# Optimization experiments

Measured on AMD Instinct MI355X. Metric: run time of the kernel, lower is better.

## Reference

```python
import jax, jax.numpy as jnp
import numpy as np

DEPTH, E, F, H, U, I, B = 12, 256, 128, 8, 1000, 1000, 64
HD = E // H  # head dim = 32
N = 2 * F + 1  # seq len = 257


def _ln(x, g, b, eps=1e-5):
    m = jnp.mean(x, axis=-1, keepdims=True)
    v = jnp.var(x, axis=-1, keepdims=True)
    return (x - m) / jnp.sqrt(v + eps) * g + b


def setup_inputs() -> dict:
    key = jax.random.key(0)
    ks = jax.random.split(key, 16)
    s = 0.02  # weight scale for numeric sanity
    inp = {
        "user": jax.random.randint(ks[0], (B, 1), 0, U, dtype=jnp.int64) if jax.config.jax_enable_x64 else jax.random.randint(ks[0], (B, 1), 0, U).astype(jnp.int32),
        "item": jax.random.randint(ks[1], (B, 1), 0, I).astype(jnp.int32),
        "user_table": jax.random.normal(ks[2], (E, U, F), jnp.float32) * s,
        "item_table": jax.random.normal(ks[3], (E, I, F), jnp.float32) * s,
        "cls_token": jax.random.normal(ks[4], (1, 1, E), jnp.float32),
        "positions": jax.random.normal(ks[5], (N, E), jnp.float32) * s,
        "ln1_g": jnp.ones((DEPTH, E), jnp.float32),
        "ln1_b": jnp.zeros((DEPTH, E), jnp.float32),
        "Wq": jax.random.normal(ks[6], (DEPTH, E, E), jnp.float32) * s,
        "bq": jnp.zeros((DEPTH, E), jnp.float32),
        "Wk": jax.random.normal(ks[7], (DEPTH, E, E), jnp.float32) * s,
        "bk": jnp.zeros((DEPTH, E), jnp.float32),
        "Wv": jax.random.normal(ks[8], (DEPTH, E, E), jnp.float32) * s,
        "bv": jnp.zeros((DEPTH, E), jnp.float32),
        "Wo": jax.random.normal(ks[9], (DEPTH, E, E), jnp.float32) * s,
        "bo": jnp.zeros((DEPTH, E), jnp.float32),
        "ln2_g": jnp.ones((DEPTH, E), jnp.float32),
        "ln2_b": jnp.zeros((DEPTH, E), jnp.float32),
        "W1": jax.random.normal(ks[10], (DEPTH, E, 4 * E), jnp.float32) * s,
        "b1": jnp.zeros((DEPTH, 4 * E), jnp.float32),
        "W2": jax.random.normal(ks[11], (DEPTH, 4 * E, E), jnp.float32) * s,
        "b2": jnp.zeros((DEPTH, E), jnp.float32),
        "head_g": jnp.ones((E,), jnp.float32),
        "head_b": jnp.zeros((E,), jnp.float32),
        "head_W": jax.random.normal(ks[12], (E, 1), jnp.float32) * s,
        "head_bias": jnp.zeros((1,), jnp.float32),
    }
    return inp


def _forward(user, item, user_table, item_table, cls_token, positions,
             ln1_g, ln1_b, Wq, bq, Wk, bk, Wv, bv, Wo, bo,
             ln2_g, ln2_b, W1, b1, W2, b2, head_g, head_b, head_W, head_bias):
    uid = user[:, 0]
    iid = item[:, 0]
    b = uid.shape[0]
    # emb_size parallel embedding lookups, cat over table axis, then transpose:
    # x_user[b, f, e] = user_table[e, uid[b], f]  -> (b, F, E)
    xu = jnp.transpose(user_table[:, uid, :], (1, 2, 0))
    xi = jnp.transpose(item_table[:, iid, :], (1, 2, 0))
    cls = jnp.broadcast_to(cls_token, (b, 1, E))
    x = jnp.concatenate([cls, xu, xi], axis=1) + positions  # (b, N, E)

    def block(x, p):
        g1, be1, wq, bq_, wk, bk_, wv, bv_, wo, bo_, g2, be2, w1, bb1, w2, bb2 = p
        h = _ln(x, g1, be1)

        def heads(w, bias):
            y = h @ w + bias  # (b, N, E)
            return y.reshape(b, N, H, HD).transpose(0, 2, 1, 3)  # (b, H, N, HD)

        q, k, v = heads(wq, bq_), heads(wk, bk_), heads(wv, bv_)
        energy = jnp.einsum('bhqd,bhkd->bhqk', q, k)  # NOTE: unscaled pre-softmax
        att = jax.nn.softmax(energy, axis=-1) / jnp.sqrt(jnp.float32(E))  # post-softmax scaling quirk
        o = jnp.einsum('bhqk,bhkd->bhqd', att, v)
        o = o.transpose(0, 2, 1, 3).reshape(b, N, E)
        x = x + (o @ wo + bo_)
        h2 = _ln(x, g2, be2)
        ff = jax.nn.gelu(h2 @ w1 + bb1, approximate=False) @ w2 + bb2
        return x + ff, None

    x, _ = jax.lax.scan(block, x, (ln1_g, ln1_b, Wq, bq, Wk, bk, Wv, bv, Wo, bo,
                                   ln2_g, ln2_b, W1, b1, W2, b2))
    pooled = jnp.mean(x, axis=1)  # (b, E)
    return _ln(pooled, head_g, head_b) @ head_W + head_bias  # (b, 1)


def reference(user, item, user_table, item_table, cls_token, positions,
              ln1_g, ln1_b, Wq, bq, Wk, bk, Wv, bv, Wo, bo,
              ln2_g, ln2_b, W1, b1, W2, b2, head_g, head_b, head_W, head_bias):
    return _forward(user, item, user_table, item_table, cls_token, positions,
                    ln1_g, ln1_b, Wq, bq, Wk, bk, Wv, bv, Wo, bo,
                    ln2_g, ln2_b, W1, b1, W2, b2, head_g, head_b, head_W, head_bias)
```

## Files before the change

### kernel.cpp

```cpp
#include <hip/hip_runtime.h>
#include <hip/hip_fp16.h>
#include <math.h>

constexpr int DEPTH = 12;
constexpr int E     = 256;
constexpr int H     = 8;
constexpr int HD    = 32;
constexpr int N     = 257;
constexpr int B     = 64;
constexpr int BN    = B * N;
constexpr int FFD   = 1024;
constexpr int UCNT  = 1000;
constexpr int Fdim  = 128;

enum { EPI_RESID = 1, EPI_GELU = 2, EPI_QKV = 3 };

typedef _Float16 f16x8 __attribute__((ext_vector_type(8)));
typedef _Float16 f16x4 __attribute__((ext_vector_type(4)));
typedef float    f32x4 __attribute__((ext_vector_type(4)));

__device__ __forceinline__ float gelu_exact(float z) {
  return 0.5f * z * (1.0f + erff(z * 0.70710678118654752440f));
}

__global__ __launch_bounds__(128) void embed_kernel(
    const int* __restrict__ user, const int* __restrict__ item,
    const float* __restrict__ utab, const float* __restrict__ itab,
    const float* __restrict__ cls, const float* __restrict__ pos,
    float* __restrict__ x)
{
  const int e = blockIdx.x;
  const int b = blockIdx.y;
  const int f = threadIdx.x;
  const int uid = user[b];
  const int iid = item[b];
  const float uu = utab[((size_t)e * UCNT + uid) * Fdim + f];
  const float ii = itab[((size_t)e * UCNT + iid) * Fdim + f];
  x[((size_t)b * N + 1 + f) * E + e]        = uu + pos[(1 + f) * E + e];
  x[((size_t)b * N + 1 + Fdim + f) * E + e] = ii + pos[(1 + Fdim + f) * E + e];
  if (f == 0) x[((size_t)b * N) * E + e] = cls[e] + pos[e];
}

__global__ __launch_bounds__(256) void convT_kernel(
    const float* __restrict__ in, __half* __restrict__ out,
    int K, int NC, int NCtot, int ncoff)
{
  __shared__ float tile[32][33];
  const int tx = threadIdx.x, ty = threadIdx.y;
  const int n0 = blockIdx.x * 32, k0 = blockIdx.y * 32;
  const float* ip = in + (size_t)blockIdx.z * K * NC;
  __half* op = out + (size_t)blockIdx.z * NCtot * K;
#pragma unroll
  for (int r = 0; r < 4; ++r) {
    const int kk = ty + r * 8;
    tile[kk][tx] = ip[(size_t)(k0 + kk) * NC + n0 + tx];
  }
  __syncthreads();
#pragma unroll
  for (int r = 0; r < 4; ++r) {
    const int nn = ty + r * 8;
    op[(size_t)(ncoff + n0 + nn) * K + k0 + tx] = __float2half(tile[tx][nn]);
  }
}

__global__ __launch_bounds__(256) void ln_kernel(
    const float* __restrict__ x, __half* __restrict__ y,
    const float* __restrict__ g, const float* __restrict__ b)
{
  const int wave = threadIdx.x >> 6, lane = threadIdx.x & 63;
  const int row  = blockIdx.x * 4 + wave;
  const float4 v = *(const float4*)(x + (size_t)row * E + lane * 4);
  float s = v.x + v.y + v.z + v.w;
  float q = v.x * v.x + v.y * v.y + v.z * v.z + v.w * v.w;
#pragma unroll
  for (int o = 32; o > 0; o >>= 1) { s += __shfl_xor(s, o); q += __shfl_xor(q, o); }
  const float mean = s * (1.0f / 256.0f);
  const float var  = q * (1.0f / 256.0f) - mean * mean;
  const float rstd = rsqrtf(var + 1e-5f);
  const float4 gg = *(const float4*)(g + lane * 4);
  const float4 bb = *(const float4*)(b + lane * 4);
  __half2 h0 = __floats2half2_rn((v.x - mean) * rstd * gg.x + bb.x,
                                 (v.y - mean) * rstd * gg.y + bb.y);
  __half2 h1 = __floats2half2_rn((v.z - mean) * rstd * gg.z + bb.z,
                                 (v.w - mean) * rstd * gg.w + bb.w);
  __half2* yp = (__half2*)(y + (size_t)row * E + lane * 4);
  yp[0] = h0; yp[1] = h1;
}

template<int K, int NCOUT, int EPI>
__global__ __launch_bounds__(256) void gemm_f16(
    const __half* __restrict__ A, const __half* __restrict__ Wt,
    const float* __restrict__ b0, const float* __restrict__ b1,
    const float* __restrict__ b2, void* __restrict__ outp)
{
  __shared__ __align__(16) char smem[64 * 132 * 4];
  __half (*As)[40] = (__half(*)[40])smem;
  __half (*Ws)[40] = (__half(*)[40])(smem + 5120);
  float* Cs = (float*)smem;

  const int t    = threadIdx.x;
  const int row0 = blockIdx.y * 64;
  const int col0 = blockIdx.x * 128;
  const int wave = t >> 6, lane = t & 63;
  const int wm = (wave >> 1) * 32;
  const int wn = (wave & 1) * 64;
  const int lm = lane & 15, lq = lane >> 4;

  const int ar = t >> 2, ak = (t & 3) * 8;
  const int wr = t >> 1, wk = (t & 1) * 16;

  f32x4 acc[2][4];
#pragma unroll
  for (int i = 0; i < 2; ++i)
#pragma unroll
    for (int j = 0; j < 4; ++j) acc[i][j] = (f32x4){0.f, 0.f, 0.f, 0.f};

  for (int k0 = 0; k0 < K; k0 += 32) {
    const float4 av  = *(const float4*)(A  + (size_t)(row0 + ar) * K + k0 + ak);
    const float4 wv0 = *(const float4*)(Wt + (size_t)(col0 + wr) * K + k0 + wk);
    const float4 wv1 = *(const float4*)(Wt + (size_t)(col0 + wr) * K + k0 + wk + 8);
    __syncthreads();
    *(float4*)&As[ar][ak]      = av;
    *(float4*)&Ws[wr][wk]      = wv0;
    *(float4*)&Ws[wr][wk + 8]  = wv1;
    __syncthreads();
    f16x8 af[2], bf[4];
#pragma unroll
    for (int mt = 0; mt < 2; ++mt)
      af[mt] = *(const f16x8*)&As[wm + mt * 16 + lm][lq * 8];
#pragma unroll
    for (int nt = 0; nt < 4; ++nt)
      bf[nt] = *(const f16x8*)&Ws[wn + nt * 16 + lm][lq * 8];
#pragma unroll
    for (int mt = 0; mt < 2; ++mt)
#pragma unroll
      for (int nt = 0; nt < 4; ++nt)
        acc[mt][nt] = __builtin_amdgcn_mfma_f32_16x16x32_f16(af[mt], bf[nt], acc[mt][nt], 0, 0, 0);
  }

  __syncthreads();
#pragma unroll
  for (int mt = 0; mt < 2; ++mt)
#pragma unroll
    for (int nt = 0; nt < 4; ++nt) {
      const int cc = wn + nt * 16 + lm;
#pragma unroll
      for (int r = 0; r < 4; ++r) {
        const int rr = wm + mt * 16 + lq * 4 + r;
        Cs[rr * 132 + cc] = acc[mt][nt][r];
      }
    }
  __syncthreads();

#pragma unroll
  for (int i = 0; i < 4; ++i) {
    const int flat = i * 2048 + t * 8;
    const int row = flat >> 7, col = flat & 127;
    const int token = row0 + row;
    const int cg = col0 + col;
    float v[8];
    *(float4*)&v[0] = *(const float4*)&Cs[row * 132 + col];
    *(float4*)&v[4] = *(const float4*)&Cs[row * 132 + col + 4];

    if (EPI == EPI_QKV) {
      const int tsel = cg >> 8;
      const int rc   = cg & 255;
      const float* bp = (tsel == 0) ? b0 : (tsel == 1 ? b1 : b2);
#pragma unroll
      for (int j = 0; j < 8; ++j) v[j] += bp[rc + j];
      const unsigned tu = (unsigned)token;
      const unsigned bb = tu / 257u;
      const unsigned nn = tu - bb * 257u;
      const int hh = rc >> 5, d0 = rc & 31;
      __half* dst = (__half*)outp + (size_t)tsel * (BN * 256)
                  + (((size_t)bb * H + hh) * N + nn) * HD + d0;
      __align__(16) __half hv[8];
#pragma unroll
      for (int j = 0; j < 8; ++j) hv[j] = __float2half(v[j]);
      *(float4*)dst = *(const float4*)hv;
    } else if (EPI == EPI_GELU) {
#pragma unroll
      for (int j = 0; j < 8; ++j) v[j] = gelu_exact(v[j] + b0[cg + j]);
      __align__(16) __half hv[8];
#pragma unroll
      for (int j = 0; j < 8; ++j) hv[j] = __float2half(v[j]);
      *(float4*)((__half*)outp + (size_t)token * NCOUT + cg) = *(const float4*)hv;
    } else {
      float* xo = (float*)outp + (size_t)token * 256 + cg;
      const float4 x0 = *(const float4*)xo;
      const float4 x1 = *(const float4*)(xo + 4);
      v[0] += b0[cg + 0] + x0.x; v[1] += b0[cg + 1] + x0.y;
      v[2] += b0[cg + 2] + x0.z; v[3] += b0[cg + 3] + x0.w;
      v[4] += b0[cg + 4] + x1.x; v[5] += b0[cg + 5] + x1.y;
      v[6] += b0[cg + 6] + x1.z; v[7] += b0[cg + 7] + x1.w;
      *(float4*)xo       = *(const float4*)&v[0];
      *(float4*)(xo + 4) = *(const float4*)&v[4];
    }
  }
}

__global__ __launch_bounds__(256) void attn_mfma(
    const __half* __restrict__ q, const __half* __restrict__ k,
    const __half* __restrict__ v, __half* __restrict__ o)
{
  __shared__ __align__(16) __half Ks[272][40];
  __shared__ __align__(16) __half Vt[32][280];

  const int bh = blockIdx.x;
  const int chunk = blockIdx.y;
  const int bb = bh >> 3, hh = bh & 7;
  const int t = threadIdx.x;
  const int wave = t >> 6, lane = t & 63;
  const int lm = lane & 15, lq = lane >> 4;

  const __half* kg = k + (size_t)bh * N * HD;
  const __half* vg = v + (size_t)bh * N * HD;

  const f16x8 zero8 = {0, 0, 0, 0, 0, 0, 0, 0};
  for (int i = t; i < 272 * 4; i += 256) {
    const int n = i >> 2, c8 = (i & 3) * 8;
    f16x8 kv = zero8, vv = zero8;
    if (n < N) {
      kv = *(const f16x8*)(kg + (size_t)n * HD + c8);
      vv = *(const f16x8*)(vg + (size_t)n * HD + c8);
    }
    *(f16x8*)&Ks[n][c8] = kv;
#pragma unroll
    for (int j = 0; j < 8; ++j) Vt[c8 + j][n] = vv[j];
  }
  __syncthreads();

  const int ntiles = chunk ? 8 : 9;
  const int tbase  = chunk ? 9 : 0;
  for (int ti = wave; ti < ntiles; ti += 4) {
    const int q0 = (tbase + ti) * 16;
    const int qg = q0 + lm;
    const int qrow = (qg < N) ? qg : (N - 1);
    const f16x8 bq = *(const f16x8*)(q + ((size_t)bh * N + qrow) * HD + lq * 8);
    f32x4 Ot0 = {0.f, 0.f, 0.f, 0.f}, Ot1 = {0.f, 0.f, 0.f, 0.f};
    float mm = -3.0e38f, ll = 0.0f;

    for (int kt = 0; kt < 17; ++kt) {
      const int k0 = kt * 16;
      const f16x8 ak = *(const f16x8*)&Ks[k0 + lm][lq * 8];
      f32x4 s = __builtin_amdgcn_mfma_f32_16x16x32_f16(ak, bq, (f32x4){0.f, 0.f, 0.f, 0.f}, 0, 0, 0);
      if (k0 == 256) {
        if (lq != 0) s[0] = -3.0e38f;
        s[1] = -3.0e38f; s[2] = -3.0e38f; s[3] = -3.0e38f;
      }
      float tm = fmaxf(fmaxf(s[0], s[1]), fmaxf(s[2], s[3]));
      tm = fmaxf(tm, __shfl_xor(tm, 16));
      tm = fmaxf(tm, __shfl_xor(tm, 32));
      const float mn    = fmaxf(mm, tm);
      const float alpha = __expf(mm - mn);
      const float p0 = __expf(s[0] - mn);
      const float p1 = __expf(s[1] - mn);
      const float p2 = __expf(s[2] - mn);
      const float p3 = __expf(s[3] - mn);
      float ts = p0 + p1 + p2 + p3;
      ts += __shfl_xor(ts, 16);
      ts += __shfl_xor(ts, 32);
      ll = ll * alpha + ts;
      Ot0 *= alpha;
      Ot1 *= alpha;
      const f16x4 pb = {(_Float16)p0, (_Float16)p1, (_Float16)p2, (_Float16)p3};
      const f16x4 av0 = *(const f16x4*)&Vt[lm][k0 + lq * 4];
      const f16x4 av1 = *(const f16x4*)&Vt[16 + lm][k0 + lq * 4];
      Ot0 = __builtin_amdgcn_mfma_f32_16x16x16f16(av0, pb, Ot0, 0, 0, 0);
      Ot1 = __builtin_amdgcn_mfma_f32_16x16x16f16(av1, pb, Ot1, 0, 0, 0);
      mm = mn;
    }

    const float inv = 1.0f / (16.0f * ll);
    if (qg < N) {
      __half* op = o + ((size_t)bb * N + qg) * E + hh * HD + lq * 4;
      __half2* p0 = (__half2*)op;
      p0[0] = __floats2half2_rn(Ot0[0] * inv, Ot0[1] * inv);
      p0[1] = __floats2half2_rn(Ot0[2] * inv, Ot0[3] * inv);
      __half2* p1 = (__half2*)(op + 16);
      p1[0] = __floats2half2_rn(Ot1[0] * inv, Ot1[1] * inv);
      p1[1] = __floats2half2_rn(Ot1[2] * inv, Ot1[3] * inv);
    }
  }
}

__global__ __launch_bounds__(256) void head_kernel(
    const float* __restrict__ x, const float* __restrict__ g,
    const float* __restrict__ bb, const float* __restrict__ hw,
    const float* __restrict__ hbias, float* __restrict__ out)
{
  const int b = blockIdx.x;
  const int e = threadIdx.x;
  const float* xp = x + (size_t)b * N * E + e;
  float s = 0.0f;
  for (int n = 0; n < N; ++n) s += xp[(size_t)n * E];
  const float p = s / 257.0f;

  float ls = p, lq = p * p;
#pragma unroll
  for (int o = 32; o > 0; o >>= 1) { ls += __shfl_xor(ls, o); lq += __shfl_xor(lq, o); }
  __shared__ float sm[4], sv[4], sd[4];
  const int wv = e >> 6, ln = e & 63;
  if (ln == 0) { sm[wv] = ls; sv[wv] = lq; }
  __syncthreads();
  const float mean = (sm[0] + sm[1] + sm[2] + sm[3]) * (1.0f / 256.0f);
  const float var  = (sv[0] + sv[1] + sv[2] + sv[3]) * (1.0f / 256.0f) - mean * mean;
  const float y = (p - mean) * rsqrtf(var + 1e-5f) * g[e] + bb[e];
  float d = y * hw[e];
#pragma unroll
  for (int o = 32; o > 0; o >>= 1) d += __shfl_xor(d, o);
  if (ln == 0) sd[wv] = d;
  __syncthreads();
  if (e == 0) out[b] = sd[0] + sd[1] + sd[2] + sd[3] + hbias[0];
}

extern "C" void kernel_launch(void* const* d_in, const int* in_sizes, int n_in,
                              void* d_out, int out_size, void* d_ws, size_t ws_size,
                              hipStream_t stream)
{
  const int*   user = (const int*)d_in[0];
  const int*   item = (const int*)d_in[1];
  const float* utab = (const float*)d_in[2];
  const float* itab = (const float*)d_in[3];
  const float* cls  = (const float*)d_in[4];
  const float* pos  = (const float*)d_in[5];
  const float* ln1g = (const float*)d_in[6];
  const float* ln1b = (const float*)d_in[7];
  const float* Wq   = (const float*)d_in[8];
  const float* bq   = (const float*)d_in[9];
  const float* Wk   = (const float*)d_in[10];
  const float* bk   = (const float*)d_in[11];
  const float* Wv   = (const float*)d_in[12];
  const float* bv   = (const float*)d_in[13];
  const float* Wo   = (const float*)d_in[14];
  const float* bo   = (const float*)d_in[15];
  const float* ln2g = (const float*)d_in[16];
  const float* ln2b = (const float*)d_in[17];
  const float* W1   = (const float*)d_in[18];
  const float* b1   = (const float*)d_in[19];
  const float* W2   = (const float*)d_in[20];
  const float* b2   = (const float*)d_in[21];
  const float* hg   = (const float*)d_in[22];
  const float* hb   = (const float*)d_in[23];
  const float* hW   = (const float*)d_in[24];
  const float* hbias= (const float*)d_in[25];
  float* out = (float*)d_out;

  float*  x  = (float*)d_ws;
  __half* h  = (__half*)(x + (size_t)BN * E);
  __half* fq = h + (size_t)BN * E;
  __half* Wqkvt = fq + (size_t)BN * FFD;
  __half* Wot   = Wqkvt + (size_t)DEPTH * 768 * 256;
  __half* W1t   = Wot   + (size_t)DEPTH * 256 * 256;
  __half* W2t   = W1t   + (size_t)DEPTH * 1024 * 256;
  __half* qb = fq;
  __half* kb = fq + (size_t)BN * 256;
  __half* vb = fq + (size_t)2 * BN * 256;

  convT_kernel<<<dim3(8, 8, DEPTH),  dim3(32, 8), 0, stream>>>(Wq, Wqkvt, 256, 256, 768, 0);
  convT_kernel<<<dim3(8, 8, DEPTH),  dim3(32, 8), 0, stream>>>(Wk, Wqkvt, 256, 256, 768, 256);
  convT_kernel<<<dim3(8, 8, DEPTH),  dim3(32, 8), 0, stream>>>(Wv, Wqkvt, 256, 256, 768, 512);
  convT_kernel<<<dim3(8, 8, DEPTH),  dim3(32, 8), 0, stream>>>(Wo, Wot, 256, 256, 256, 0);
  convT_kernel<<<dim3(32, 8, DEPTH), dim3(32, 8), 0, stream>>>(W1, W1t, 256, 1024, 1024, 0);
  convT_kernel<<<dim3(8, 32, DEPTH), dim3(32, 8), 0, stream>>>(W2, W2t, 1024, 256, 256, 0);

  embed_kernel<<<dim3(E, B), 128, 0, stream>>>(user, item, utab, itab, cls, pos, x);

  for (int L = 0; L < DEPTH; ++L) {
    ln_kernel<<<BN / 4, 256, 0, stream>>>(x, h, ln1g + L * E, ln1b + L * E);
    gemm_f16<256, 768, EPI_QKV><<<dim3(6, 257), 256, 0, stream>>>(
        h, Wqkvt + (size_t)L * 768 * 256, bq + L * E, bk + L * E, bv + L * E, fq);
    attn_mfma<<<dim3(512, 2), 256, 0, stream>>>(qb, kb, vb, h);
    gemm_f16<256, 256, EPI_RESID><<<dim3(2, 257), 256, 0, stream>>>(
        h, Wot + (size_t)L * 256 * 256, bo + L * E, bo + L * E, bo + L * E, x);
    ln_kernel<<<BN / 4, 256, 0, stream>>>(x, h, ln2g + L * E, ln2b + L * E);
    gemm_f16<256, 1024, EPI_GELU><<<dim3(8, 257), 256, 0, stream>>>(
        h, W1t + (size_t)L * 1024 * 256, b1 + L * FFD, b1 + L * FFD, b1 + L * FFD, fq);
    gemm_f16<1024, 256, EPI_RESID><<<dim3(2, 257), 256, 0, stream>>>(
        fq, W2t + (size_t)L * 256 * 1024, b2 + L * E, b2 + L * E, b2 + L * E, x);
  }

  head_kernel<<<B, 256, 0, stream>>>(x, hg, hb, hW, hbias, out);
}
```

Measured before the change: 1.973 ms.

## Restructure GEMM with direct global-to-LDS loads, swizzled tiles, larger token tiles

The GEMM kernel is rebuilt so that the weight matrix is the M side (128 columns) and tokens are the N side. Tokens are tiled 128 per block for QKV and FFN1 and 64 per block for the residual GEMMs. Tiles are loaded with global_load_lds straight into XOR-swizzled LDS, and the epilogue writes from registers with no C staging through shared memory. The token buffer is padded to 16512 rows, and a new kernel zeroes the pad so the 128-token tiles can read past BN. The embedding kernel is also rewritten to use a shared-memory transpose for coalesced access. The aim is more MFMA work per loaded byte and less LDS traffic, at the cost of more accumulator registers and a K loop that loads and computes without overlap, with two barriers per step.

```diff
diff --git a/kernel.cpp b/kernel.cpp
--- a/kernel.cpp
+++ b/kernel.cpp
@@ -9,6 +9,7 @@
 constexpr int N     = 257;
 constexpr int B     = 64;
 constexpr int BN    = B * N;
+constexpr int BNP   = 16512;
 constexpr int FFD   = 1024;
 constexpr int UCNT  = 1000;
 constexpr int Fdim  = 128;
@@ -23,22 +24,50 @@
   return 0.5f * z * (1.0f + erff(z * 0.70710678118654752440f));
 }
 
-__global__ __launch_bounds__(128) void embed_kernel(
+#define GLOAD_LDS16(g, l) __builtin_amdgcn_global_load_lds( \
+    (const __attribute__((address_space(1))) void*)(g),     \
+    (__attribute__((address_space(3))) void*)(l), 16, 0, 0)
+
+__global__ __launch_bounds__(256) void embed_kernel(
     const int* __restrict__ user, const int* __restrict__ item,
     const float* __restrict__ utab, const float* __restrict__ itab,
+    const float* __restrict__ pos, float* __restrict__ x)
+{
+  __shared__ float tile[32][33];
+  const int tx = threadIdx.x, ty = threadIdx.y;
+  const int b  = blockIdx.z;
+  const int e0 = blockIdx.x * 32;
+  const int ft = blockIdx.y;
+  const bool isU = (ft < 4);
+  const int f0 = (ft & 3) * 32;
+  const int id = isU ? user[b] : item[b];
+  const float* tab = isU ? utab : itab;
+  const int nbase = isU ? 1 : 1 + Fdim;
+#pragma unroll
+  for (int r = 0; r < 4; ++r) {
+    const int e = ty + r * 8;
+    tile[e][tx] = tab[((size_t)(e0 + e) * UCNT + id) * Fdim + f0 + tx];
+  }
+  __syncthreads();
+#pragma unroll
+  for (int r = 0; r < 4; ++r) {
+    const int f = ty + r * 8;
+    const int n = nbase + f0 + f;
+    x[((size_t)b * N + n) * E + e0 + tx] = tile[tx][f] + pos[(size_t)n * E + e0 + tx];
+  }
+}
+
+__global__ __launch_bounds__(256) void cls_pad_kernel(
     const float* __restrict__ cls, const float* __restrict__ pos,
-    float* __restrict__ x)
-{
-  const int e = blockIdx.x;
-  const int b = blockIdx.y;
-  const int f = threadIdx.x;
-  const int uid = user[b];
-  const int iid = item[b];
-  const float uu = utab[((size_t)e * UCNT + uid) * Fdim + f];
-  const float ii = itab[((size_t)e * UCNT + iid) * Fdim + f];
-  x[((size_t)b * N + 1 + f) * E + e]        = uu + pos[(1 + f) * E + e];
-  x[((size_t)b * N + 1 + Fdim + f) * E + e] = ii + pos[(1 + Fdim + f) * E + e];
-  if (f == 0) x[((size_t)b * N) * E + e] = cls[e] + pos[e];
+    float* __restrict__ x, __half* __restrict__ h)
+{
+  const int t = blockIdx.x * 256 + threadIdx.x;
+  if (blockIdx.y == 0) {
+    const int b = t >> 8, e = t & 255;
+    x[((size_t)b * N) * E + e] = cls[e] + pos[e];
+  } else {
+    h[(size_t)BN * E + t] = __float2half(0.0f);
+  }
 }
 
 __global__ __launch_bounds__(256) void convT_kernel(
@@ -87,114 +116,143 @@
   yp[0] = h0; yp[1] = h1;
 }
 
-template<int K, int NCOUT, int EPI>
+template<int BMC, int BNT, int K, int NCOUT, int EPI>
 __global__ __launch_bounds__(256) void gemm_f16(
-    const __half* __restrict__ A, const __half* __restrict__ Wt,
+    const __half* __restrict__ Act, const __half* __restrict__ Wt,
     const float* __restrict__ b0, const float* __restrict__ b1,
     const float* __restrict__ b2, void* __restrict__ outp)
 {
-  __shared__ __align__(16) char smem[64 * 132 * 4];
-  __half (*As)[40] = (__half(*)[40])smem;
-  __half (*Ws)[40] = (__half(*)[40])(smem + 5120);
-  float* Cs = (float*)smem;
-
-  const int t    = threadIdx.x;
-  const int row0 = blockIdx.y * 64;
-  const int col0 = blockIdx.x * 128;
+  static_assert(BMC == 128, "col tile fixed at 128");
+  constexpr int NT  = BNT / 32;
+  constexpr int BSEG = BNT / 16;
+  constexpr int BPW  = BSEG / 4;
+
+  __shared__ __half Ws[128 * 32];
+  __shared__ __half Bs[BNT * 32];
+
+  const int t = threadIdx.x;
   const int wave = t >> 6, lane = t & 63;
-  const int wm = (wave >> 1) * 32;
-  const int wn = (wave & 1) * 64;
   const int lm = lane & 15, lq = lane >> 4;
-
-  const int ar = t >> 2, ak = (t & 3) * 8;
-  const int wr = t >> 1, wk = (t & 1) * 16;
-
-  f32x4 acc[2][4];
-#pragma unroll
-  for (int i = 0; i < 2; ++i)
-#pragma unroll
-    for (int j = 0; j < 4; ++j) acc[i][j] = (f32x4){0.f, 0.f, 0.f, 0.f};
+  const int col0 = blockIdx.x * BMC;
+  const int tok0 = blockIdx.y * BNT;
+
+  const int srow = lane >> 2, sp = lane & 3;
+  const __half* wg[2]; __half* wl[2];
+#pragma unroll
+  for (int i = 0; i < 2; ++i) {
+    const int seg = wave * 2 + i;
+    const int row = seg * 16 + srow;
+    const int slot = sp ^ ((row >> 1) & 3);
+    wg[i] = Wt + (size_t)(col0 + row) * K + slot * 8;
+    wl[i] = &Ws[seg * 512];
+  }
+  const __half* ag[BPW]; __half* al[BPW];
+#pragma unroll
+  for (int i = 0; i < BPW; ++i) {
+    const int seg = wave * BPW + i;
+    const int row = seg * 16 + srow;
+    const int slot = sp ^ ((row >> 1) & 3);
+    ag[i] = Act + (size_t)(tok0 + row) * K + slot * 8;
+    al[i] = &Bs[seg * 512];
+  }
+
+  const int wm = (wave >> 1) * 64;
+  const int wn = (wave & 1) * (BNT / 2);
+
+  f32x4 acc[4][NT];
+#pragma unroll
+  for (int i = 0; i < 4; ++i)
+#pragma unroll
+    for (int j = 0; j < NT; ++j) acc[i][j] = (f32x4){0.f, 0.f, 0.f, 0.f};
 
   for (int k0 = 0; k0 < K; k0 += 32) {
-    const float4 av  = *(const float4*)(A  + (size_t)(row0 + ar) * K + k0 + ak);
-    const float4 wv0 = *(const float4*)(Wt + (size_t)(col0 + wr) * K + k0 + wk);
-    const float4 wv1 = *(const float4*)(Wt + (size_t)(col0 + wr) * K + k0 + wk + 8);
+#pragma unroll
+    for (int i = 0; i < 2; ++i)   GLOAD_LDS16(wg[i] + k0, wl[i]);
+#pragma unroll
+    for (int i = 0; i < BPW; ++i) GLOAD_LDS16(ag[i] + k0, al[i]);
     __syncthreads();
-    *(float4*)&As[ar][ak]      = av;
-    *(float4*)&Ws[wr][wk]      = wv0;
-    *(float4*)&Ws[wr][wk + 8]  = wv1;
+
+    f16x8 af[4], bf[NT];
+#pragma unroll
+    for (int mt = 0; mt < 4; ++mt) {
+      const int row = wm + mt * 16 + lm;
+      af[mt] = *(const f16x8*)&Ws[row * 32 + (lq ^ ((row >> 1) & 3)) * 8];
+    }
+#pragma unroll
+    for (int nt = 0; nt < NT; ++nt) {
+      const int row = wn + nt * 16 + lm;
+      bf[nt] = *(const f16x8*)&Bs[row * 32 + (lq ^ ((row >> 1) & 3)) * 8];
+    }
+#pragma unroll
+    for (int mt = 0; mt < 4; ++mt)
+#pragma unroll
+      for (int nt = 0; nt < NT; ++nt)
+        acc[mt][nt] = __builtin_amdgcn_mfma_f32_16x16x32_f16(af[mt], bf[nt], acc[mt][nt], 0, 0, 0);
     __syncthreads();
-    f16x8 af[2], bf[4];
-#pragma unroll
-    for (int mt = 0; mt < 2; ++mt)
-      af[mt] = *(const f16x8*)&As[wm + mt * 16 + lm][lq * 8];
-#pragma unroll
-    for (int nt = 0; nt < 4; ++nt)
-      bf[nt] = *(const f16x8*)&Ws[wn + nt * 16 + lm][lq * 8];
-#pragma unroll
-    for (int mt = 0; mt < 2; ++mt)
-#pragma unroll
-      for (int nt = 0; nt < 4; ++nt)
-        acc[mt][nt] = __builtin_amdgcn_mfma_f32_16x16x32_f16(af[mt], bf[nt], acc[mt][nt], 0, 0, 0);
-  }
-
-  __syncthreads();
-#pragma unroll
-  for (int mt = 0; mt < 2; ++mt)
-#pragma unroll
-    for (int nt = 0; nt < 4; ++nt) {
-      const int cc = wn + nt * 16 + lm;
-#pragma unroll
-      for (int r = 0; r < 4; ++r) {
-        const int rr = wm + mt * 16 + lq * 4 + r;
-        Cs[rr * 132 + cc] = acc[mt][nt][r];
+  }
+
+  float br[4][4];
+#pragma unroll
+  for (int mt = 0; mt < 4; ++mt) {
+    const int cg = col0 + wm + mt * 16 + lq * 4;
+    const float* bp;
+    if constexpr (EPI == EPI_QKV) {
+      const int tsel = cg >> 8;
+      bp = (tsel == 0) ? b0 : (tsel == 1 ? b1 : b2);
+      bp += (cg & 255);
+    } else {
+      bp = b0 + cg;
+    }
+    const float4 bv = *(const float4*)bp;
+    br[mt][0] = bv.x; br[mt][1] = bv.y; br[mt][2] = bv.z; br[mt][3] = bv.w;
+  }
+
+#pragma unroll
+  for (int nt = 0; nt < NT; ++nt) {
+    const int token = tok0 + wn + nt * 16 + lm;
+    if constexpr (EPI == EPI_RESID) {
+      float* xrow = (float*)outp + (size_t)token * 256;
+#pragma unroll
+      for (int mt = 0; mt < 4; ++mt) {
+        const int cg = col0 + wm + mt * 16 + lq * 4;
+        float4 xv = *(float4*)(xrow + cg);
+        xv.x += acc[mt][nt][0] + br[mt][0];
+        xv.y += acc[mt][nt][1] + br[mt][1];
+        xv.z += acc[mt][nt][2] + br[mt][2];
+        xv.w += acc[mt][nt][3] + br[mt][3];
+        *(float4*)(xrow + cg) = xv;
       }
-    }
-  __syncthreads();
-
-#pragma unroll
-  for (int i = 0; i < 4; ++i) {
-    const int flat = i * 2048 + t * 8;
-    const int row = flat >> 7, col = flat & 127;
-    const int token = row0 + row;
-    const int cg = col0 + col;
-    float v[8];
-    *(float4*)&v[0] = *(const float4*)&Cs[row * 132 + col];
-    *(float4*)&v[4] = *(const float4*)&Cs[row * 132 + col + 4];
-
-    if (EPI == EPI_QKV) {
-      const int tsel = cg >> 8;
-      const int rc   = cg & 255;
-      const float* bp = (tsel == 0) ? b0 : (tsel == 1 ? b1 : b2);
-#pragma unroll
-      for (int j = 0; j < 8; ++j) v[j] += bp[rc + j];
-      const unsigned tu = (unsigned)token;
-      const unsigned bb = tu / 257u;
-      const unsigned nn = tu - bb * 257u;
-      const int hh = rc >> 5, d0 = rc & 31;
-      __half* dst = (__half*)outp + (size_t)tsel * (BN * 256)
-                  + (((size_t)bb * H + hh) * N + nn) * HD + d0;
-      __align__(16) __half hv[8];
-#pragma unroll
-      for (int j = 0; j < 8; ++j) hv[j] = __float2half(v[j]);
-      *(float4*)dst = *(const float4*)hv;
-    } else if (EPI == EPI_GELU) {
-#pragma unroll
-      for (int j = 0; j < 8; ++j) v[j] = gelu_exact(v[j] + b0[cg + j]);
-      __align__(16) __half hv[8];
-#pragma unroll
-      for (int j = 0; j < 8; ++j) hv[j] = __float2half(v[j]);
-      *(float4*)((__half*)outp + (size_t)token * NCOUT + cg) = *(const float4*)hv;
+    } else if constexpr (EPI == EPI_GELU) {
+      if (token < BN) {
+        __half* orow = (__half*)outp + (size_t)token * NCOUT;
+#pragma unroll
+        for (int mt = 0; mt < 4; ++mt) {
+          const int cg = col0 + wm + mt * 16 + lq * 4;
+          f16x4 hv;
+#pragma unroll
+          for (int r = 0; r < 4; ++r)
+            hv[r] = (_Float16)gelu_exact(acc[mt][nt][r] + br[mt][r]);
+          *(f16x4*)(orow + cg) = hv;
+        }
+      }
     } else {
-      float* xo = (float*)outp + (size_t)token * 256 + cg;
-      const float4 x0 = *(const float4*)xo;
-      const float4 x1 = *(const float4*)(xo + 4);
-      v[0] += b0[cg + 0] + x0.x; v[1] += b0[cg + 1] + x0.y;
-      v[2] += b0[cg + 2] + x0.z; v[3] += b0[cg + 3] + x0.w;
-      v[4] += b0[cg + 4] + x1.x; v[5] += b0[cg + 5] + x1.y;
-      v[6] += b0[cg + 6] + x1.z; v[7] += b0[cg + 7] + x1.w;
-      *(float4*)xo       = *(const float4*)&v[0];
-      *(float4*)(xo + 4) = *(const float4*)&v[4];
+      if (token < BN) {
+        const unsigned tu = (unsigned)token;
+        const unsigned bb = tu / 257u;
+        const unsigned nn = tu - bb * 257u;
+#pragma unroll
+        for (int mt = 0; mt < 4; ++mt) {
+          const int cg = col0 + wm + mt * 16 + lq * 4;
+          const int tsel = cg >> 8, rc = cg & 255;
+          __half* dst = (__half*)outp + (size_t)tsel * (BN * 256)
+                      + (((size_t)bb * H + (rc >> 5)) * N + nn) * HD + (rc & 31);
+          f16x4 hv;
+#pragma unroll
+          for (int r = 0; r < 4; ++r)
+            hv[r] = (_Float16)(acc[mt][nt][r] + br[mt][r]);
+          *(f16x4*)dst = hv;
+        }
+      }
     }
   }
 }
@@ -348,7 +406,7 @@
 
   float*  x  = (float*)d_ws;
   __half* h  = (__half*)(x + (size_t)BN * E);
-  __half* fq = h + (size_t)BN * E;
+  __half* fq = h + (size_t)BNP * E;
   __half* Wqkvt = fq + (size_t)BN * FFD;
   __half* Wot   = Wqkvt + (size_t)DEPTH * 768 * 256;
   __half* W1t   = Wot   + (size_t)DEPTH * 256 * 256;
@@ -364,19 +422,20 @@
   convT_kernel<<<dim3(32, 8, DEPTH), dim3(32, 8), 0, stream>>>(W1, W1t, 256, 1024, 1024, 0);
   convT_kernel<<<dim3(8, 32, DEPTH), dim3(32, 8), 0, stream>>>(W2, W2t, 1024, 256, 256, 0);
 
-  embed_kernel<<<dim3(E, B), 128, 0, stream>>>(user, item, utab, itab, cls, pos, x);
+  cls_pad_kernel<<<dim3(64, 2), 256, 0, stream>>>(cls, pos, x, h);
+  embed_kernel<<<dim3(8, 8, B), dim3(32, 8), 0, stream>>>(user, item, utab, itab, pos, x);
 
   for (int L = 0; L < DEPTH; ++L) {
     ln_kernel<<<BN / 4, 256, 0, stream>>>(x, h, ln1g + L * E, ln1b + L * E);
-    gemm_f16<256, 768, EPI_QKV><<<dim3(6, 257), 256, 0, stream>>>(
+    gemm_f16<128, 128, 256, 768, EPI_QKV><<<dim3(6, 129), 256, 0, stream>>>(
         h, Wqkvt + (size_t)L * 768 * 256, bq + L * E, bk + L * E, bv + L * E, fq);
     attn_mfma<<<dim3(512, 2), 256, 0, stream>>>(qb, kb, vb, h);
-    gemm_f16<256, 256, EPI_RESID><<<dim3(2, 257), 256, 0, stream>>>(
+    gemm_f16<128, 64, 256, 256, EPI_RESID><<<dim3(2, 257), 256, 0, stream>>>(
         h, Wot + (size_t)L * 256 * 256, bo + L * E, bo + L * E, bo + L * E, x);
     ln_kernel<<<BN / 4, 256, 0, stream>>>(x, h, ln2g + L * E, ln2b + L * E);
-    gemm_f16<256, 1024, EPI_GELU><<<dim3(8, 257), 256, 0, stream>>>(
-        h, W1t + (size_t)L * 1024 * 256, b1 + L * FFD, b1 + L * FFD, b1 + L * FFD, fq);
-    gemm_f16<1024, 256, EPI_RESID><<<dim3(2, 257), 256, 0, stream>>>(
+    gemm_f16<128, 128, 256, 1024, EPI_GELU><<<dim3(8, 129), 256, 0, stream>>>(
+        h, W1t + (size_t)L * 1024 * 256, b1 + (size_t)L * FFD, b1 + (size_t)L * FFD, b1 + (size_t)L * FFD, fq);
+    gemm_f16<128, 64, 1024, 256, EPI_RESID><<<dim3(2, 257), 256, 0, stream>>>(
         fq, W2t + (size_t)L * 256 * 1024, b2 + L * E, b2 + L * E, b2 + L * E, x);
   }
 
```

New measurement: 1.753 ms. 1.13x faster.
